# Optimization experiments

Hardware: AMD Instinct MI355X
Metric: run time of the kernel (lower is better)

Reference implementation:

```python
import jax, jax.numpy as jnp
import numpy as np

H, DK, DV, CHUNK = 4, 256, 256, 32

def _silu(x):
    return x * jax.nn.sigmoid(x)

def _l2norm(x, eps=1e-6):
    return x * jax.lax.rsqrt(jnp.sum(x * x, -1, keepdims=True) + eps)

def _rmsnorm(x, w, eps=1e-5):
    return x * jax.lax.rsqrt(jnp.mean(x * x, -1, keepdims=True) + eps) * w

def _causal_dwconv(x, w):
    # x: (B, L, C), w: (C, K) -> causal depthwise conv -> (B, L, C)
    C = x.shape[-1]
    K = w.shape[-1]
    xp = jnp.pad(x, ((0, 0), (K - 1, 0), (0, 0))).transpose(0, 2, 1)  # NCH
    y = jax.lax.conv_general_dilated(xp, w[:, None, :], (1,), 'VALID',
                                     feature_group_count=C,
                                     dimension_numbers=('NCH', 'OIH', 'NCH'))
    return y.transpose(0, 2, 1)

def _fir(x, filt):
    # x: (B, L, H, D), filt: (H, D, K) depthwise causal FIR per (head, channel)
    B, L, h, d = x.shape
    y = _causal_dwconv(x.reshape(B, L, h * d), filt.reshape(h * d, -1))
    return y.reshape(B, L, h, d)

def _delta_rule_chunkwise(q, k, v, beta):
    # q,k: (B,H,L,DK); v: (B,H,L,DV); beta: (B,H,L). L % CHUNK == 0.
    b, h, L, dk = q.shape
    dv = v.shape[-1]
    n = L // CHUNK
    q = _l2norm(q)
    k = _l2norm(k)
    v = v * beta[..., None]
    k_beta = k * beta[..., None]
    rs = lambda t: t.reshape(b, h, n, CHUNK, -1)
    q, k, v, k_beta = rs(q), rs(k), rs(v), rs(k_beta)
    eye = jnp.eye(CHUNK, dtype=q.dtype)
    strict_lower = jnp.tril(jnp.ones((CHUNK, CHUNK), bool), -1)
    A = jnp.where(strict_lower, jnp.einsum('bhncd,bhnsd->bhncs', k_beta, k), 0.0)
    # The torch row-wise loop computes (I + strict_lower(K_beta K^T))^{-1}
    attn_inv = jax.scipy.linalg.solve_triangular(eye + A, jnp.broadcast_to(eye, A.shape), lower=True)
    u = attn_inv @ v       # (b,h,n,c,dv)
    w = attn_inv @ k_beta  # (b,h,n,c,dk)
    incl_lower = jnp.tril(jnp.ones((CHUNK, CHUNK), bool))

    def step(S, inp):
        q_i, k_i, u_i, w_i = inp
        attn_local = jnp.where(incl_lower, q_i @ jnp.swapaxes(k_i, -1, -2), 0.0)
        u_t = u_i - w_i @ S
        o_i = q_i @ S + attn_local @ u_t
        return S + jnp.swapaxes(k_i, -1, -2) @ u_t, o_i

    S0 = jnp.zeros((b, h, dk, dv), q.dtype)
    xs = tuple(jnp.moveaxis(t, 2, 0) for t in (q, k, u, w))
    S, out = jax.lax.scan(step, S0, xs)
    return jnp.moveaxis(out, 0, 2).reshape(b, h, L, dv), S

def _stats(x):
    # per-branch head statistics over feature dim: mean, var, abs-mean, l2-norm
    return jnp.stack([x.mean(-1), x.var(-1), jnp.abs(x).mean(-1),
                      jnp.sqrt(jnp.sum(x * x, -1))], -1)

def _forward(x, Wq, Wk, Wv, Wb, conv_q, conv_k, conv_v, fir_long, fir_short,
             W1, b1, W2, b2, log_temp, base_bias, conv_residual_logit, rms_w, Wo):
    B, L, D = x.shape
    q = _silu(_causal_dwconv(x @ Wq, conv_q)).reshape(B, L, H, DK)
    k = _silu(_causal_dwconv(x @ Wk, conv_k)).reshape(B, L, H, DK)
    v = _silu(_causal_dwconv(x @ Wv, conv_v)).reshape(B, L, H, DV)
    beta = jax.nn.sigmoid(x @ Wb)  # (B, L, H)
    delta, _S = _delta_rule_chunkwise(q.transpose(0, 2, 1, 3), k.transpose(0, 2, 1, 3),
                                      v.transpose(0, 2, 1, 3), beta.transpose(0, 2, 1))
    delta = delta.transpose(0, 2, 1, 3)  # (B, L, H, DV)
    f_short = _fir(v, fir_short)
    f_long = _fir(v, fir_long)
    stats = jnp.concatenate([_stats(f_short), _stats(f_long), _stats(delta), _stats(v)], -1)
    hidden_exp = jnp.broadcast_to(x[:, :, None, :], (B, L, H, D))
    gate_in = jnp.concatenate([hidden_exp, stats], -1)  # (B,L,H,D+16)
    h1 = jax.nn.gelu(gate_in @ W1 + b1, approximate=False)
    logits = h1 @ W2 + b2 + base_bias  # (B, L, H, 4)
    temp = jax.nn.softplus(log_temp) + 1e-4
    p = jax.nn.softmax(logits / temp[:, None], -1)
    eps = 0.05  # step 0 -> alpha = 1 -> floor = floor_start
    p = jnp.maximum(p, jnp.array([eps, eps, 0.0, 0.0], p.dtype))
    p = p / jnp.sum(p, -1, keepdims=True)
    o = (p[..., 0:1] * f_short + p[..., 1:2] * f_long +
         p[..., 2:3] * delta + p[..., 3:4] * v)
    o = o + 0.5 * jax.nn.sigmoid(conv_residual_logit)[None, None, :, None] * f_short
    o = _rmsnorm(o, rms_w)
    return o.reshape(B, L, H * DV) @ Wo

def setup_inputs():
    key = jax.random.key(0)
    ks = jax.random.split(key, 13)
    B, L, D = 2, 2048, 1024
    f = jnp.float32
    n = lambda k, shape, s=0.02: jax.random.normal(k, shape, f) * s
    return {
        'x': jax.random.normal(ks[0], (B, L, D), f),
        'Wq': n(ks[1], (D, D)),
        'Wk': n(ks[2], (D, D)),
        'Wv': n(ks[3], (D, D)),
        'Wb': n(ks[4], (D, H)),
        'conv_q': n(ks[5], (D, 4), 0.1),
        'conv_k': n(ks[6], (D, 4), 0.1),
        'conv_v': n(ks[7], (D, 4), 0.1),
        'fir_long': n(ks[8], (H, DV, 64)),
        'fir_short': n(ks[9], (H, DV, 5)),
        'W1': n(ks[10], (D + 16, D)),
        'b1': jnp.zeros((D,), f),
        'W2': n(ks[11], (D, 4)),
        'b2': jnp.zeros((4,), f),
        'log_temp': jnp.full((H,), float(np.log(np.expm1(0.7))), f),
        'base_bias': jnp.tile(jnp.array([-0.5, -0.5, 1.0, 3.0], f), (H, 1)),
        'conv_residual_logit': jnp.full((H,), -2.0, f),
        'rms_w': jnp.ones((DV,), f),
        'Wo': n(ks[12], (D, D)),
    }

def reference(x, Wq, Wk, Wv, Wb, conv_q, conv_k, conv_v, fir_long, fir_short,
              W1, b1, W2, b2, log_temp, base_bias, conv_residual_logit, rms_w, Wo):
    return _forward(x, Wq, Wk, Wv, Wb, conv_q, conv_k, conv_v, fir_long, fir_short,
                    W1, b1, W2, b2, log_temp, base_bias, conv_residual_logit, rms_w, Wo)
```

## Files before the change

### kernel.cpp

```cpp
#include <hip/hip_runtime.h>
#include <math.h>

constexpr int NB = 2, NL = 2048, ND = 1024, NH = 4;
constexpr int NCHK = 64;
constexpr int NBL = NB * NL;
#define BLDSZ (NB * NL * ND)

constexpr int OPS_CH = 36864;
constexpr int STG_CH = 26624;

__device__ float g_v[BLDSZ];
__device__ float g_delta[BLDSZ];
__device__ float g_fs[BLDSZ];
__device__ float g_fl[BLDSZ];
__device__ float g_xw1[BLDSZ];
__device__ float g_beta[NBL * NH];
__device__ unsigned short g_qlb[BLDSZ];
__device__ unsigned short g_klb[BLDSZ];
__device__ unsigned short g_vlb[BLDSZ];
__device__ unsigned short g_ops[(size_t)8 * 64 * OPS_CH];
__device__ unsigned short g_xb[BLDSZ];
__device__ unsigned short g_omixb[BLDSZ];
__device__ unsigned short g_btw[5 * 1024 * 1024];

__device__ __forceinline__ float sigmoidf(float x) { return 1.f / (1.f + expf(-x)); }

__device__ __forceinline__ unsigned short f2bf(float f) {
  union { float f; unsigned int u; } v; v.f = f;
  unsigned int r = v.u + 0x7FFFu + ((v.u >> 16) & 1u);
  return (unsigned short)(r >> 16);
}
__device__ __forceinline__ float bf2f(unsigned int bits16) {
  union { unsigned int u; float f; } v; v.u = bits16 << 16; return v.f;
}
__device__ __forceinline__ unsigned int packbf(float a, float b) {
  return (unsigned int)f2bf(a) | ((unsigned int)f2bf(b) << 16);
}

typedef __attribute__((ext_vector_type(8))) short short8v;
typedef __attribute__((ext_vector_type(16))) float f32x16;

__device__ __forceinline__ unsigned int cvtpk(float lo, float hi) {
  unsigned int r;
  asm("v_cvt_pk_bf16_f32 %0, %1, %2" : "=v"(r) : "v"(lo), "v"(hi));
  return r;
}

__device__ __forceinline__ void mkfrag(const f32x16 v, short8v& fb0, short8v& fb1) {
  unsigned int P0 = cvtpk(v[0], v[1]),   P1 = cvtpk(v[2], v[3]);
  unsigned int P2 = cvtpk(v[4], v[5]),   P3 = cvtpk(v[6], v[7]);
  unsigned int P4 = cvtpk(v[8], v[9]),   P5 = cvtpk(v[10], v[11]);
  unsigned int P6 = cvtpk(v[12], v[13]), P7 = cvtpk(v[14], v[15]);
  asm("v_permlane32_swap_b32 %0, %1" : "+v"(P0), "+v"(P2));
  asm("v_permlane32_swap_b32 %0, %1" : "+v"(P1), "+v"(P3));
  asm("v_permlane32_swap_b32 %0, %1" : "+v"(P4), "+v"(P6));
  asm("v_permlane32_swap_b32 %0, %1" : "+v"(P5), "+v"(P7));
  unsigned int f0[4] = {P0, P1, P2, P3}, f1[4] = {P4, P5, P6, P7};
  fb0 = *(short8v*)f0; fb1 = *(short8v*)f1;
}

#define GLL16(SRC, DST)                                                                    \
  __builtin_amdgcn_global_load_lds(                                                        \
      (const __attribute__((address_space(1))) unsigned int*)(SRC),                        \
      (__attribute__((address_space(3))) unsigned int*)(DST), 16, 0, 0)

__device__ __forceinline__ void gemm128_core(const unsigned short* __restrict__ A,
                                             const unsigned short* __restrict__ Bt,
                                             int m0, int n0, int t,
                                             unsigned short* As, unsigned short* Bs,
                                             f32x16 acc[2][2]) {
  const int w = t >> 6, lane = t & 63, l31 = lane & 31, lhi = lane >> 5;
  const int wm = (w & 1) * 64, wn = (w >> 1) * 64;
#pragma unroll
  for (int mt = 0; mt < 2; ++mt)
#pragma unroll
    for (int nt = 0; nt < 2; ++nt)
#pragma unroll
      for (int e = 0; e < 16; ++e) acc[mt][nt][e] = 0.f;

  for (int k0 = 0; k0 < 1024; k0 += 64) {
#pragma unroll
    for (int i = 0; i < 4; ++i) {
      int sl = i * 4 + w;
      int srow = sl * 8 + (lane >> 3);
      int gc = (((lane & 7) ^ (srow & 7))) * 8;
      GLL16(A + (size_t)(m0 + srow) * 1024 + k0 + gc, &As[sl * 512]);
      GLL16(Bt + (size_t)(n0 + srow) * 1024 + k0 + gc, &Bs[sl * 512]);
    }
    __syncthreads();
#pragma unroll
    for (int ksl = 0; ksl < 4; ++ksl) {
      int kb = ksl * 2 + lhi;
      short8v af[2], bf[2];
#pragma unroll
      for (int mt = 0; mt < 2; ++mt) {
        int row = wm + mt * 32 + l31;
        af[mt] = *(const short8v*)&As[row * 64 + ((kb ^ (row & 7)) * 8)];
      }
#pragma unroll
      for (int nt = 0; nt < 2; ++nt) {
        int row = wn + nt * 32 + l31;
        bf[nt] = *(const short8v*)&Bs[row * 64 + ((kb ^ (row & 7)) * 8)];
      }
#pragma unroll
      for (int mt = 0; mt < 2; ++mt)
#pragma unroll
        for (int nt = 0; nt < 2; ++nt)
          acc[mt][nt] = __builtin_amdgcn_mfma_f32_32x32x16_bf16(af[mt], bf[nt], acc[mt][nt], 0, 0, 0);
    }
    __syncthreads();
  }
}

__global__ __launch_bounds__(256) void pack_all_kernel(const float* __restrict__ x,
                                                       const float* __restrict__ Wq,
                                                       const float* __restrict__ Wk,
                                                       const float* __restrict__ Wv,
                                                       const float* __restrict__ W1,
                                                       const float* __restrict__ Wo,
                                                       const float* __restrict__ Wb) {
  __shared__ float tile[64][65];
  int blk = blockIdx.x, t = threadIdx.x;
  if (blk < 2048) {
    int i8 = blk * 256 + t;
    const float* p = x + (size_t)i8 * 8;
    float4 a = *(const float4*)p;
    float4 b = *(const float4*)(p + 4);
    uint4 v;
    v.x = packbf(a.x, a.y); v.y = packbf(a.z, a.w);
    v.z = packbf(b.x, b.y); v.w = packbf(b.z, b.w);
    *(uint4*)&g_xb[(size_t)i8 * 8] = v;
    return;
  }
  if (blk < 3328) {
    int sel = (blk - 2048) >> 8, wb = (blk - 2048) & 255;
    const float* W = (sel == 0) ? Wq : (sel == 1) ? Wk : (sel == 2) ? Wv : (sel == 3) ? W1 : Wo;
    int bx = wb & 15, by = wb >> 4;
    int n0 = bx * 64, k0 = by * 64;
#pragma unroll
    for (int i = 0; i < 4; ++i) {
      int id = t + i * 256;
      int r = id >> 4, c4 = (id & 15) * 4;
      float4 v = *(const float4*)&W[(size_t)(k0 + r) * 1024 + n0 + c4];
      tile[r][c4 + 0] = v.x; tile[r][c4 + 1] = v.y; tile[r][c4 + 2] = v.z; tile[r][c4 + 3] = v.w;
    }
    __syncthreads();
    unsigned int* out = (unsigned int*)g_btw + (size_t)sel * 524288;
#pragma unroll
    for (int i = 0; i < 8; ++i) {
      int id = t + i * 256;
      int nn = id >> 5, ku = id & 31;
      out[(size_t)(n0 + nn) * 512 + (k0 >> 1) + ku] = packbf(tile[2 * ku][nn], tile[2 * ku + 1][nn]);
    }
    return;
  }
  int bl = blk - 3328;
  int h = t >> 6, lane = t & 63;
  const float* xr = x + (size_t)bl * ND;
  float acc = 0.f;
  for (int d = lane; d < ND; d += 64) acc += xr[d] * Wb[d * 4 + h];
#pragma unroll
  for (int off = 32; off; off >>= 1) acc += __shfl_xor(acc, off);
  if (lane == 0) g_beta[bl * 4 + h] = sigmoidf(acc);
}

__global__ __launch_bounds__(256) void qkv_gemm_kernel() {
  __shared__ unsigned short As[128 * 64];
  __shared__ unsigned short Bs[128 * 64];
  const int sel = blockIdx.x >> 8, hb = blockIdx.x & 255;
  const unsigned short* Bt = g_btw + (size_t)sel * 1024 * 1024;
  unsigned short* C = (sel == 0) ? g_qlb : (sel == 1) ? g_klb : g_vlb;
  const int m0 = (hb >> 3) * 128, n0 = (hb & 7) * 128;
  const int t = threadIdx.x;
  const int w = t >> 6, lane = t & 63, l31 = lane & 31, lhi = lane >> 5;
  const int wm = (w & 1) * 64, wn = (w >> 1) * 64;
  f32x16 acc[2][2];
  gemm128_core(g_xb, Bt, m0, n0, t, As, Bs, acc);
#pragma unroll
  for (int mt = 0; mt < 2; ++mt)
#pragma unroll
    for (int nt = 0; nt < 2; ++nt) {
      int col = n0 + wn + nt * 32 + l31;
#pragma unroll
      for (int e = 0; e < 16; ++e) {
        int row = m0 + wm + mt * 32 + (e & 3) + 8 * (e >> 2) + 4 * lhi;
        C[(size_t)row * 1024 + col] = f2bf(acc[mt][nt][e]);
      }
    }
}

__global__ __launch_bounds__(256) void convv_kernel(const float* __restrict__ cv) {
  int blk = blockIdx.x, t = threadIdx.x;
  int idx = blk * 256 + t;
  int c = idx & (ND - 1);
  int bl = idx >> 10;
  int l = bl & (NL - 1);
  float w0 = cv[c * 4 + 0], w1 = cv[c * 4 + 1], w2 = cv[c * 4 + 2], w3 = cv[c * 4 + 3];
  float acc = w3 * bf2f(g_vlb[(size_t)bl * ND + c]);
  if (l >= 1) acc += w2 * bf2f(g_vlb[(size_t)(bl - 1) * ND + c]);
  if (l >= 2) acc += w1 * bf2f(g_vlb[(size_t)(bl - 2) * ND + c]);
  if (l >= 3) acc += w0 * bf2f(g_vlb[(size_t)(bl - 3) * ND + c]);
  g_v[idx] = acc * sigmoidf(acc);
}

__global__ __launch_bounds__(256) void hgemm_out_kernel(float* __restrict__ Cext) {
  __shared__ unsigned short As[128 * 64];
  __shared__ unsigned short Bs[128 * 64];
  const int m0 = (blockIdx.x >> 3) * 128, n0 = (blockIdx.x & 7) * 128;
  const int t = threadIdx.x;
  const int w = t >> 6, lane = t & 63, l31 = lane & 31, lhi = lane >> 5;
  const int wm = (w & 1) * 64, wn = (w >> 1) * 64;
  f32x16 acc[2][2];
  gemm128_core(g_omixb, g_btw + (size_t)4 * 1024 * 1024, m0, n0, t, As, Bs, acc);
#pragma unroll
  for (int mt = 0; mt < 2; ++mt)
#pragma unroll
    for (int nt = 0; nt < 2; ++nt) {
      int col = n0 + wn + nt * 32 + l31;
#pragma unroll
      for (int e = 0; e < 16; ++e) {
        int row = m0 + wm + mt * 32 + (e & 3) + 8 * (e >> 2) + 4 * lhi;
        Cext[(size_t)row * 1024 + col] = acc[mt][nt][e];
      }
    }
}

__global__ __launch_bounds__(256) void delta_prep_kernel(const float* __restrict__ cq,
                                                         const float* __restrict__ ck) {
  __shared__ float X[32][260];
  __shared__ float Y[32][260];
  __shared__ float Am[32][33];
  __shared__ float Tm[32][33];
  __shared__ float bet[32];
  int blk = blockIdx.x;
  int n = blk & 63, h = (blk >> 6) & 3, b = blk >> 8;
  int t = threadIdx.x;
  size_t rowbase = (size_t)(b * NL + n * 32);
  size_t obase = (size_t)blk * OPS_CH;
  const int st_ = t >> 5, j_ = (t >> 4) & 1, lh_ = (t >> 3) & 1, e_ = t & 7;
  const int l31_ = t & 31;

  {
    const int hcol = h * 256 + t;
    const unsigned short* qp = g_qlb + hcol;
    const unsigned short* kp = g_klb + hcol;
    float wq0 = cq[hcol * 4 + 0], wq1 = cq[hcol * 4 + 1], wq2 = cq[hcol * 4 + 2], wq3 = cq[hcol * 4 + 3];
    float wk0 = ck[hcol * 4 + 0], wk1 = ck[hcol * 4 + 1], wk2 = ck[hcol * 4 + 2], wk3 = ck[hcol * 4 + 3];
    float qa = 0.f, qb_ = 0.f, qc = 0.f, ka = 0.f, kb_ = 0.f, kc = 0.f;
    if (n > 0) {
      qa = bf2f(qp[(rowbase - 3) * 1024]); qb_ = bf2f(qp[(rowbase - 2) * 1024]); qc = bf2f(qp[(rowbase - 1) * 1024]);
      ka = bf2f(kp[(rowbase - 3) * 1024]); kb_ = bf2f(kp[(rowbase - 2) * 1024]); kc = bf2f(kp[(rowbase - 1) * 1024]);
    }
#pragma unroll 4
    for (int r = 0; r < 32; ++r) {
      float qd = bf2f(qp[(rowbase + r) * 1024]);
      float kd = bf2f(kp[(rowbase + r) * 1024]);
      float aq = wq3 * qd + wq2 * qc + wq1 * qb_ + wq0 * qa;
      float ak = wk3 * kd + wk2 * kc + wk1 * kb_ + wk0 * ka;
      X[r][t] = aq * sigmoidf(aq);
      Y[r][t] = ak * sigmoidf(ak);
      qa = qb_; qb_ = qc; qc = qd;
      ka = kb_; kb_ = kc; kc = kd;
    }
  }
  if (t < 32) bet[t] = g_beta[(rowbase + t) * 4 + h];
  __syncthreads();

  {
    int wv = t >> 6, lane = t & 63;
    int r = wv * 8 + (lane >> 3), sub = lane & 7;
    float sq = 0.f, sk = 0.f;
#pragma unroll
    for (int m4 = 0; m4 < 8; ++m4) {
      float4 a = *(const float4*)&X[r][sub * 32 + m4 * 4];
      float4 bb = *(const float4*)&Y[r][sub * 32 + m4 * 4];
      sq += a.x * a.x + a.y * a.y + a.z * a.z + a.w * a.w;
      sk += bb.x * bb.x + bb.y * bb.y + bb.z * bb.z + bb.w * bb.w;
    }
    sq += __shfl_xor(sq, 1); sq += __shfl_xor(sq, 2); sq += __shfl_xor(sq, 4);
    sk += __shfl_xor(sk, 1); sk += __shfl_xor(sk, 2); sk += __shfl_xor(sk, 4);
    float rq = rsqrtf(sq + 1e-6f), rk = rsqrtf(sk + 1e-6f);
#pragma unroll
    for (int m4 = 0; m4 < 8; ++m4) {
      float4 a = *(const float4*)&X[r][sub * 32 + m4 * 4];
      a.x *= rq; a.y *= rq; a.z *= rq; a.w *= rq;
      *(float4*)&X[r][sub * 32 + m4 * 4] = a;
      float4 bb = *(const float4*)&Y[r][sub * 32 + m4 * 4];
      bb.x *= rk; bb.y *= rk; bb.z *= rk; bb.w *= rk;
      *(float4*)&Y[r][sub * 32 + m4 * 4] = bb;
    }
  }
  __syncthreads();

  if (t < 64) {
    const int al = t & 31, ah = t >> 5;
    f32x16 Cat;
#pragma unroll
    for (int e = 0; e < 16; ++e) Cat[e] = 0.f;
#pragma unroll
    for (int st = 0; st < 16; ++st) {
      int kb = st * 16 + ah * 8;
      float4 a0 = *(const float4*)&X[al][kb], a1 = *(const float4*)&X[al][kb + 4];
      float4 b0 = *(const float4*)&Y[al][kb], b1 = *(const float4*)&Y[al][kb + 4];
      unsigned int af[4] = {cvtpk(a0.x, a0.y), cvtpk(a0.z, a0.w), cvtpk(a1.x, a1.y), cvtpk(a1.z, a1.w)};
      unsigned int bf_[4] = {cvtpk(b0.x, b0.y), cvtpk(b0.z, b0.w), cvtpk(b1.x, b1.y), cvtpk(b1.z, b1.w)};
      Cat = __builtin_amdgcn_mfma_f32_32x32x16_bf16(*(short8v*)af, *(short8v*)bf_, Cat, 0, 0, 0);
    }
#pragma unroll
    for (int e = 0; e < 16; ++e) {
      int row = (e & 3) + 8 * (e >> 2) + 4 * ah, col = al;
      float v = (col <= row) ? Cat[e] : 0.f;
      g_ops[obase + 32768 + (size_t)(((col >> 4) * 64) + ((col >> 3) & 1) * 32 + row) * 8 + (col & 7)] = f2bf(v);
    }
  }

  {
    size_t qb = obase + 8192 + (size_t)(((st_ * 2 + j_) * 64) + lh_ * 32) * 8 + e_;
#pragma unroll 8
    for (int r = 0; r < 32; ++r)
      g_ops[qb + r * 8] = f2bf(X[r][t]);
#pragma unroll
    for (int j = 0; j < 2; ++j)
#pragma unroll
      for (int lh = 0; lh < 2; ++lh) {
        int kr0 = j * 16 + lh * 8;
        uint4 v;
        v.x = packbf(Y[kr0 + 0][t], Y[kr0 + 1][t]);
        v.y = packbf(Y[kr0 + 2][t], Y[kr0 + 3][t]);
        v.z = packbf(Y[kr0 + 4][t], Y[kr0 + 5][t]);
        v.w = packbf(Y[kr0 + 6][t], Y[kr0 + 7][t]);
        *(uint4*)&g_ops[obase + 16384 + (size_t)(((st_ * 2 + j) * 64) + lh * 32 + l31_) * 8] = v;
      }
  }
  __syncthreads();

#pragma unroll
  for (int i = 0; i < 8; ++i) {
    int j = t + i * 256;
    int r = j >> 6, d4 = (j & 63) << 2;
    float be = bet[r];
    float4 bb = *(const float4*)&Y[r][d4];
    bb.x *= be; bb.y *= be; bb.z *= be; bb.w *= be;
    *(float4*)&X[r][d4] = bb;
  }
  __syncthreads();

  if (t < 64) {
    const int al = t & 31, ah = t >> 5;
    f32x16 Cam;
#pragma unroll
    for (int e = 0; e < 16; ++e) Cam[e] = 0.f;
#pragma unroll
    for (int st = 0; st < 16; ++st) {
      int kb = st * 16 + ah * 8;
      float4 a0 = *(const float4*)&X[al][kb], a1 = *(const float4*)&X[al][kb + 4];
      float4 b0 = *(const float4*)&Y[al][kb], b1 = *(const float4*)&Y[al][kb + 4];
      unsigned int af[4] = {cvtpk(a0.x, a0.y), cvtpk(a0.z, a0.w), cvtpk(a1.x, a1.y), cvtpk(a1.z, a1.w)};
      unsigned int bf_[4] = {cvtpk(b0.x, b0.y), cvtpk(b0.z, b0.w), cvtpk(b1.x, b1.y), cvtpk(b1.z, b1.w)};
      Cam = __builtin_amdgcn_mfma_f32_32x32x16_bf16(*(short8v*)af, *(short8v*)bf_, Cam, 0, 0, 0);
    }
#pragma unroll
    for (int e = 0; e < 16; ++e) {
      int row = (e & 3) + 8 * (e >> 2) + 4 * ah, col = al;
      if (col < row) Am[row][col] = Cam[e];
    }
  }
  __syncthreads();

  if (t < 32) {
    const int j = t;
#pragma unroll
    for (int i = 0; i < 32; ++i) {
      float a = (i == j) ? 1.f : 0.f;
#pragma unroll
      for (int m = 0; m < i; ++m) {
        float p = Am[i][m] * Tm[m][j];
        a -= (m >= j) ? p : 0.f;
      }
      Tm[i][j] = a;
    }
  }
  __syncthreads();

  {
    float acc[32];
#pragma unroll
    for (int r = 0; r < 32; ++r) acc[r] = 0.f;
#pragma unroll
    for (int m = 0; m < 32; ++m) {
      float xv = X[m][t];
#pragma unroll
      for (int r = m; r < 32; ++r) acc[r] += Tm[r][m] * xv;
    }
    size_t wb = obase + (size_t)(((st_ * 2 + j_) * 64) + lh_ * 32) * 8 + e_;
#pragma unroll 8
    for (int r = 0; r < 32; ++r)
      g_ops[wb + r * 8] = f2bf(acc[r]);
  }
#pragma unroll
  for (int i = 0; i < 8; ++i) {
    int j = t + i * 256;
    int r = j >> 6, d4 = (j & 63) << 2;
    size_t gi = (rowbase + r) * ND + h * 256 + d4;
    float be = bet[r];
    float4 vv = *(const float4*)&g_v[gi];
    vv.x *= be; vv.y *= be; vv.z *= be; vv.w *= be;
    *(float4*)&Y[r][d4] = vv;
  }
  __syncthreads();

  {
    float acc[32];
#pragma unroll
    for (int r = 0; r < 32; ++r) acc[r] = 0.f;
#pragma unroll
    for (int m = 0; m < 32; ++m) {
      float yv = Y[m][t];
#pragma unroll
      for (int r = m; r < 32; ++r) acc[r] += Tm[r][m] * yv;
    }
    int q = t >> 5;
#pragma unroll
    for (int g = 0; g < 4; ++g)
#pragma unroll
      for (int lh = 0; lh < 2; ++lh) {
        int kr0 = 8 * g + 4 * lh;
        uint2 v;
        v.x = packbf(acc[kr0 + 0], acc[kr0 + 1]);
        v.y = packbf(acc[kr0 + 2], acc[kr0 + 3]);
        *(uint2*)&g_ops[obase + 24576 + (size_t)(((q * 4 + g) * 64) + lh * 32 + l31_) * 4] = v;
      }
  }
}

__global__ __launch_bounds__(256, 1) void scan_fir_kernel(const float* __restrict__ firl,
                                                          const float* __restrict__ firs) {
  __shared__ __align__(16) unsigned char smem[2 * STG_CH * 2];
  const int blk = blockIdx.x;
  const int t = threadIdx.x;

  if (blk < 64) {
    if (t >= 64) return;
    unsigned short (*buf)[STG_CH] = (unsigned short (*)[STG_CH])smem;
    const int bh = blk & 7;
    const int b = bh >> 2, h = bh & 3;
    const int s = blk >> 3;
    const int lane = t;
    const int l31 = lane & 31, lhi = lane >> 5;

    f32x16 Sacc[8];
#pragma unroll
    for (int st = 0; st < 8; ++st)
#pragma unroll
      for (int e = 0; e < 16; ++e) Sacc[st][e] = 0.f;

    const unsigned short* ops = g_ops + (size_t)bh * 64 * OPS_CH;
    const int fo = lane * 8;
    const int utg = 24576 + s * 1024;

#define STAGE_CHUNK(SRC, DST)                                                              \
    {                                                                                      \
      const unsigned short* sp = (SRC);                                                    \
      unsigned short* dp = (DST);                                                          \
      _Pragma("unroll")                                                                    \
      for (int k = 0; k < 48; ++k)                                                         \
        GLL16(sp + (size_t)k * 512 + fo, dp + k * 512);                                    \
      _Pragma("unroll")                                                                    \
      for (int k = 0; k < 2; ++k) {                                                        \
        GLL16(sp + utg + (size_t)k * 512 + fo, dp + 24576 + k * 512);                      \
        GLL16(sp + 32768 + (size_t)k * 512 + fo, dp + 25600 + k * 512);                    \
      }                                                                                    \
    }

    STAGE_CHUNK(ops, &buf[0][0]);

    for (int n = 0; n < 64; ++n) {
      const int cur = n & 1;
      if (n == 0) asm volatile("s_waitcnt vmcnt(0)" ::: "memory");
      else        asm volatile("s_waitcnt vmcnt(16)" ::: "memory");

      if (n < 63) STAGE_CHUNK(ops + (size_t)(n + 1) * OPS_CH, &buf[cur ^ 1][0]);

      const unsigned short* Lb = &buf[cur][0];
      f32x16 wuA, wuB, ooA, ooB;
#pragma unroll
      for (int e = 0; e < 16; ++e) { wuA[e] = 0.f; wuB[e] = 0.f; ooA[e] = 0.f; ooB[e] = 0.f; }

#pragma unroll
      for (int st = 0; st < 8; ++st) {
        short8v s0, s1;
        mkfrag(Sacc[st], s0, s1);
        short8v wa0 = *(const short8v*)&Lb[(st * 2 + 0) * 512 + fo];
        short8v wa1 = *(const short8v*)&Lb[(st * 2 + 1) * 512 + fo];
        short8v qa0 = *(const short8v*)&Lb[8192 + (st * 2 + 0) * 512 + fo];
        short8v qa1 = *(const short8v*)&Lb[8192 + (st * 2 + 1) * 512 + fo];
        wuA = __builtin_amdgcn_mfma_f32_32x32x16_bf16(wa0, s0, wuA, 0, 0, 0);
        wuB = __builtin_amdgcn_mfma_f32_32x32x16_bf16(wa1, s1, wuB, 0, 0, 0);
        ooA = __builtin_amdgcn_mfma_f32_32x32x16_bf16(qa0, s0, ooA, 0, 0, 0);
        ooB = __builtin_amdgcn_mfma_f32_32x32x16_bf16(qa1, s1, ooB, 0, 0, 0);
      }

      f32x16 ut;
#pragma unroll
      for (int g = 0; g < 4; ++g) {
        uint2 uu = *(const uint2*)&Lb[24576 + ((g * 64) + lhi * 32 + l31) * 4];
        ut[4 * g + 0] = bf2f(uu.x & 0xffffu) - wuA[4 * g + 0] - wuB[4 * g + 0];
        ut[4 * g + 1] = bf2f(uu.x >> 16)     - wuA[4 * g + 1] - wuB[4 * g + 1];
        ut[4 * g + 2] = bf2f(uu.y & 0xffffu) - wuA[4 * g + 2] - wuB[4 * g + 2];
        ut[4 * g + 3] = bf2f(uu.y >> 16)     - wuA[4 * g + 3] - wuB[4 * g + 3];
      }
      short8v u0, u1;
      mkfrag(ut, u0, u1);

      {
        short8v aa0 = *(const short8v*)&Lb[25600 + 0 * 512 + fo];
        short8v aa1 = *(const short8v*)&Lb[25600 + 1 * 512 + fo];
        ooA = __builtin_amdgcn_mfma_f32_32x32x16_bf16(aa0, u0, ooA, 0, 0, 0);
        ooB = __builtin_amdgcn_mfma_f32_32x32x16_bf16(aa1, u1, ooB, 0, 0, 0);
      }
#pragma unroll
      for (int st = 0; st < 8; ++st) {
        short8v ka0 = *(const short8v*)&Lb[16384 + (st * 2 + 0) * 512 + fo];
        short8v ka1 = *(const short8v*)&Lb[16384 + (st * 2 + 1) * 512 + fo];
        Sacc[st] = __builtin_amdgcn_mfma_f32_32x32x16_bf16(ka0, u0, Sacc[st], 0, 0, 0);
        Sacc[st] = __builtin_amdgcn_mfma_f32_32x32x16_bf16(ka1, u1, Sacc[st], 0, 0, 0);
      }

      size_t ob = ((size_t)(b * NL + n * 32)) * ND + h * 256 + s * 32 + l31;
#pragma unroll
      for (int e = 0; e < 16; ++e) {
        int row = (e & 3) + 8 * (e >> 2) + 4 * lhi;
        g_delta[ob + (size_t)row * ND] = ooA[e] + ooB[e];
      }
    }
#undef STAGE_CHUNK
  } else if (blk < 64 + 512) {
    float (*ft)[257] = (float (*)[257])smem;
    int fb_ = blk - 64;
    int cbk = fb_ & 3, lb = (fb_ >> 2) & 63, b = fb_ >> 8;
    int c = cbk * 256 + t;
    const float* fbp = firl + (size_t)cbk * 256 * 64;
#pragma unroll 4
    for (int i = 0; i < 64; ++i) {
      int j = t + i * 256;
      ft[j & 63][j >> 6] = fbp[j];
    }
    __syncthreads();
    float ff[64];
#pragma unroll
    for (int i = 0; i < 64; ++i) ff[i] = ft[i][t];
    float acc[32];
#pragma unroll
    for (int i = 0; i < 32; ++i) acc[i] = 0.f;
    const float* vb = g_v + (size_t)b * NL * ND + c;
    const int l0 = lb * 32;
#pragma unroll
    for (int d = 0; d < 95; ++d) {
      int lr = l0 - 63 + d;
      float vv = (lr >= 0) ? vb[(size_t)lr * ND] : 0.f;
      const int lo = (d > 63) ? (d - 63) : 0;
      const int hi = (d < 31) ? d : 31;
#pragma unroll
      for (int li = lo; li <= hi; ++li) acc[li] += ff[d - li] * vv;
    }
    float* ob = g_fl + ((size_t)(b * NL + l0)) * ND + c;
#pragma unroll
    for (int li = 0; li < 32; ++li) ob[(size_t)li * ND] = acc[li];
  } else if (blk < 64 + 512 + BLDSZ / 1024) {
    int idx4 = (blk - 576) * 256 + t;
    int c4 = idx4 & 255;
    int bl = idx4 >> 8;
    int l = bl & (NL - 1);
    float fw[4][5];
#pragma unroll
    for (int j = 0; j < 4; ++j)
#pragma unroll
      for (int tap = 0; tap < 5; ++tap) fw[j][tap] = firs[(c4 * 4 + j) * 5 + tap];
    float4 acc = {0.f, 0.f, 0.f, 0.f};
    const float4* v4 = (const float4*)g_v;
#pragma unroll
    for (int tap = 0; tap < 5; ++tap) {
      int ls = l + tap - 4;
      if (ls >= 0) {
        float4 vv = v4[(size_t)(bl + tap - 4) * 256 + c4];
        acc.x += fw[0][tap] * vv.x; acc.y += fw[1][tap] * vv.y;
        acc.z += fw[2][tap] * vv.z; acc.w += fw[3][tap] * vv.w;
      }
    }
    ((float4*)g_fs)[(size_t)bl * 256 + c4] = acc;
  } else {
    unsigned short* As = (unsigned short*)smem;
    unsigned short* Bs = (unsigned short*)smem + 8192;
    int hb = blk - (64 + 512 + BLDSZ / 1024);
    const int m0 = (hb >> 3) * 128, n0 = (hb & 7) * 128;
    const int w = t >> 6, lane = t & 63, l31 = lane & 31, lhi = lane >> 5;
    const int wm = (w & 1) * 64, wn = (w >> 1) * 64;
    f32x16 acc[2][2];
    gemm128_core(g_xb, g_btw + (size_t)3 * 1024 * 1024, m0, n0, t, As, Bs, acc);
#pragma unroll
    for (int mt = 0; mt < 2; ++mt)
#pragma unroll
      for (int nt = 0; nt < 2; ++nt) {
        int col = n0 + wn + nt * 32 + l31;
#pragma unroll
        for (int e = 0; e < 16; ++e) {
          int row = m0 + wm + mt * 32 + (e & 3) + 8 * (e >> 2) + 4 * lhi;
          g_xw1[(size_t)row * 1024 + col] = acc[mt][nt][e];
        }
      }
  }
}

__global__ __launch_bounds__(256) void tail_kernel(const float* __restrict__ W1,
                                                   const float* __restrict__ b1,
                                                   const float* __restrict__ W2,
                                                   const float* __restrict__ b2,
                                                   const float* __restrict__ log_temp,
                                                   const float* __restrict__ base_bias,
                                                   const float* __restrict__ crl,
                                                   const float* __restrict__ rms_w) {
  __shared__ float st[4][16];
  __shared__ float red[4][4];
  __shared__ float pl[4][4];
  int bl = blockIdx.x, t = threadIdx.x;
  int h = t >> 6, lane = t & 63;

  {
    size_t base = (size_t)bl * ND + h * 256 + lane * 4;
#pragma unroll
    for (int br = 0; br < 4; ++br) {
      const float* p = (br == 0) ? g_fs : (br == 1) ? g_fl : (br == 2) ? g_delta : g_v;
      float4 x4 = *(const float4*)&p[base];
      float s = x4.x + x4.y + x4.z + x4.w;
      float s2 = x4.x * x4.x + x4.y * x4.y + x4.z * x4.z + x4.w * x4.w;
      float sa = fabsf(x4.x) + fabsf(x4.y) + fabsf(x4.z) + fabsf(x4.w);
#pragma unroll
      for (int off = 32; off; off >>= 1) {
        s += __shfl_xor(s, off);
        s2 += __shfl_xor(s2, off);
        sa += __shfl_xor(sa, off);
      }
      if (lane == 0) {
        float mean = s * (1.f / 256.f);
        st[h][br * 4 + 0] = mean;
        st[h][br * 4 + 1] = s2 * (1.f / 256.f) - mean * mean;
        st[h][br * 4 + 2] = sa * (1.f / 256.f);
        st[h][br * 4 + 3] = sqrtf(s2);
      }
    }
  }
  __syncthreads();

  const float* W1s = W1 + 1024 * 1024;
  for (int hh = 0; hh < 4; ++hh) {
    float sv[16];
#pragma unroll
    for (int s = 0; s < 16; ++s) sv[s] = st[hh][s];
    float a0 = 0.f, a1 = 0.f, a2 = 0.f, a3 = 0.f;
    for (int j = t; j < 1024; j += 256) {
      float val = g_xw1[(size_t)bl * 1024 + j] + b1[j];
#pragma unroll
      for (int s = 0; s < 16; ++s) val += sv[s] * W1s[s * 1024 + j];
      float gg = 0.5f * val * (1.f + erff(val * 0.70710678118654752f));
      float4 w2 = *(const float4*)&W2[j * 4];
      a0 += gg * w2.x; a1 += gg * w2.y; a2 += gg * w2.z; a3 += gg * w2.w;
    }
#pragma unroll
    for (int off = 32; off; off >>= 1) {
      a0 += __shfl_xor(a0, off); a1 += __shfl_xor(a1, off);
      a2 += __shfl_xor(a2, off); a3 += __shfl_xor(a3, off);
    }
    if (lane == 0) { red[h][0] = a0; red[h][1] = a1; red[h][2] = a2; red[h][3] = a3; }
    __syncthreads();
    if (t == 0) {
      float lg[4];
#pragma unroll
      for (int m = 0; m < 4; ++m)
        lg[m] = red[0][m] + red[1][m] + red[2][m] + red[3][m] + b2[m] + base_bias[hh * 4 + m];
      float lt = log_temp[hh];
      float sp = (lt > 20.f) ? lt : log1pf(expf(lt));
      float inv = 1.f / (sp + 1e-4f);
      float z0 = lg[0] * inv, z1 = lg[1] * inv, z2 = lg[2] * inv, z3 = lg[3] * inv;
      float mx = fmaxf(fmaxf(z0, z1), fmaxf(z2, z3));
      float e0 = expf(z0 - mx), e1 = expf(z1 - mx), e2 = expf(z2 - mx), e3 = expf(z3 - mx);
      float si = 1.f / (e0 + e1 + e2 + e3);
      float p0 = e0 * si, p1 = e1 * si, p2 = e2 * si, p3 = e3 * si;
      p0 = fmaxf(p0, 0.05f); p1 = fmaxf(p1, 0.05f);
      float s2i = 1.f / (p0 + p1 + p2 + p3);
      p0 *= s2i; p1 *= s2i; p2 *= s2i; p3 *= s2i;
      p0 += 0.5f * sigmoidf(crl[hh]);
      pl[hh][0] = p0; pl[hh][1] = p1; pl[hh][2] = p2; pl[hh][3] = p3;
    }
    __syncthreads();
  }

  float p0 = pl[h][0], p1 = pl[h][1], p2 = pl[h][2], p3 = pl[h][3];
  size_t base = (size_t)bl * ND + h * 256 + lane * 4;
  float4 a = *(const float4*)&g_fs[base];
  float4 bb = *(const float4*)&g_fl[base];
  float4 c = *(const float4*)&g_delta[base];
  float4 d = *(const float4*)&g_v[base];
  float o0 = p0 * a.x + p1 * bb.x + p2 * c.x + p3 * d.x;
  float o1 = p0 * a.y + p1 * bb.y + p2 * c.y + p3 * d.y;
  float o2 = p0 * a.z + p1 * bb.z + p2 * c.z + p3 * d.z;
  float o3 = p0 * a.w + p1 * bb.w + p2 * c.w + p3 * d.w;
  float s2 = o0 * o0 + o1 * o1 + o2 * o2 + o3 * o3;
#pragma unroll
  for (int off = 32; off; off >>= 1) s2 += __shfl_xor(s2, off);
  float rms = rsqrtf(s2 * (1.f / 256.f) + 1e-5f);
  float4 w4 = *(const float4*)&rms_w[lane * 4];
  uint2 pw;
  pw.x = packbf(o0 * rms * w4.x, o1 * rms * w4.y);
  pw.y = packbf(o2 * rms * w4.z, o3 * rms * w4.w);
  *(uint2*)&g_omixb[base] = pw;
}

extern "C" void kernel_launch(void* const* d_in, const int* in_sizes, int n_in,
                              void* d_out, int out_size, void* d_ws, size_t ws_size,
                              hipStream_t stream) {
  const float* x = (const float*)d_in[0];
  const float* Wq = (const float*)d_in[1];
  const float* Wk = (const float*)d_in[2];
  const float* Wv = (const float*)d_in[3];
  const float* Wb = (const float*)d_in[4];
  const float* cq = (const float*)d_in[5];
  const float* ck = (const float*)d_in[6];
  const float* cv = (const float*)d_in[7];
  const float* firl = (const float*)d_in[8];
  const float* firs = (const float*)d_in[9];
  const float* W1 = (const float*)d_in[10];
  const float* b1 = (const float*)d_in[11];
  const float* W2 = (const float*)d_in[12];
  const float* b2 = (const float*)d_in[13];
  const float* ltp = (const float*)d_in[14];
  const float* bbs = (const float*)d_in[15];
  const float* crl = (const float*)d_in[16];
  const float* rw = (const float*)d_in[17];
  const float* Wo = (const float*)d_in[18];
  float* out = (float*)d_out;

  dim3 blk(256);
  pack_all_kernel<<<2048 + 5 * 256 + NBL, blk, 0, stream>>>(x, Wq, Wk, Wv, W1, Wo, Wb);
  qkv_gemm_kernel<<<768, blk, 0, stream>>>();
  convv_kernel<<<16384, blk, 0, stream>>>(cv);
  delta_prep_kernel<<<NB * NH * NCHK, blk, 0, stream>>>(cq, ck);
  scan_fir_kernel<<<64 + 512 + BLDSZ / 1024 + 256, blk, 0, stream>>>(firl, firs);
  tail_kernel<<<NBL, blk, 0, stream>>>(W1, b1, W2, b2, ltp, bbs, crl, rw);
  hgemm_out_kernel<<<256, blk, 0, stream>>>(out);
}
```

Before: 386.8 us.

## Swizzle GEMM block order and give each wavefront one head in tail gating

The QKV and output GEMMs remap block indices so consecutive blocks walk down M within one N column, aiming for better L2 reuse of the weight tile. The tail kernel drops the serial four-head loop with its two block barriers per head. Each wavefront now computes its own head's gate MLP and softmax independently over all 1024 hidden units, leaving a single barrier. This removes barriers and idle threads but gives each wave four times the loop iterations of the old per-head split.

```diff
diff --git a/kernel.cpp b/kernel.cpp
--- a/kernel.cpp
+++ b/kernel.cpp
@@ -167,7 +167,9 @@
 __global__ __launch_bounds__(256) void qkv_gemm_kernel() {
   __shared__ unsigned short As[128 * 64];
   __shared__ unsigned short Bs[128 * 64];
-  const int sel = blockIdx.x >> 8, hb = blockIdx.x & 255;
+  const int sel = blockIdx.x >> 8;
+  const int hb0 = blockIdx.x & 255;
+  const int hb = (hb0 & 7) * 32 + (hb0 >> 3);
   const unsigned short* Bt = g_btw + (size_t)sel * 1024 * 1024;
   unsigned short* C = (sel == 0) ? g_qlb : (sel == 1) ? g_klb : g_vlb;
   const int m0 = (hb >> 3) * 128, n0 = (hb & 7) * 128;
@@ -206,7 +208,8 @@
 __global__ __launch_bounds__(256) void hgemm_out_kernel(float* __restrict__ Cext) {
   __shared__ unsigned short As[128 * 64];
   __shared__ unsigned short Bs[128 * 64];
-  const int m0 = (blockIdx.x >> 3) * 128, n0 = (blockIdx.x & 7) * 128;
+  const int hb = (blockIdx.x & 7) * 32 + (blockIdx.x >> 3);
+  const int m0 = (hb >> 3) * 128, n0 = (hb & 7) * 128;
   const int t = threadIdx.x;
   const int w = t >> 6, lane = t & 63, l31 = lane & 31, lhi = lane >> 5;
   const int wm = (w & 1) * 64, wn = (w >> 1) * 64;
@@ -620,7 +623,6 @@
                                                    const float* __restrict__ crl,
                                                    const float* __restrict__ rms_w) {
   __shared__ float st[4][16];
-  __shared__ float red[4][4];
   __shared__ float pl[4][4];
   int bl = blockIdx.x, t = threadIdx.x;
   int h = t >> 6, lane = t & 63;
@@ -651,13 +653,13 @@
   }
   __syncthreads();
 
-  const float* W1s = W1 + 1024 * 1024;
-  for (int hh = 0; hh < 4; ++hh) {
+  {
+    const float* W1s = W1 + 1024 * 1024;
     float sv[16];
 #pragma unroll
-    for (int s = 0; s < 16; ++s) sv[s] = st[hh][s];
+    for (int s = 0; s < 16; ++s) sv[s] = st[h][s];
     float a0 = 0.f, a1 = 0.f, a2 = 0.f, a3 = 0.f;
-    for (int j = t; j < 1024; j += 256) {
+    for (int j = lane; j < 1024; j += 64) {
       float val = g_xw1[(size_t)bl * 1024 + j] + b1[j];
 #pragma unroll
       for (int s = 0; s < 16; ++s) val += sv[s] * W1s[s * 1024 + j];
@@ -670,14 +672,10 @@
       a0 += __shfl_xor(a0, off); a1 += __shfl_xor(a1, off);
       a2 += __shfl_xor(a2, off); a3 += __shfl_xor(a3, off);
     }
-    if (lane == 0) { red[h][0] = a0; red[h][1] = a1; red[h][2] = a2; red[h][3] = a3; }
-    __syncthreads();
-    if (t == 0) {
-      float lg[4];
-#pragma unroll
-      for (int m = 0; m < 4; ++m)
-        lg[m] = red[0][m] + red[1][m] + red[2][m] + red[3][m] + b2[m] + base_bias[hh * 4 + m];
-      float lt = log_temp[hh];
+    if (lane == 0) {
+      float lg[4] = {a0 + b2[0] + base_bias[h * 4 + 0], a1 + b2[1] + base_bias[h * 4 + 1],
+                     a2 + b2[2] + base_bias[h * 4 + 2], a3 + b2[3] + base_bias[h * 4 + 3]};
+      float lt = log_temp[h];
       float sp = (lt > 20.f) ? lt : log1pf(expf(lt));
       float inv = 1.f / (sp + 1e-4f);
       float z0 = lg[0] * inv, z1 = lg[1] * inv, z2 = lg[2] * inv, z3 = lg[3] * inv;
@@ -688,11 +686,11 @@
       p0 = fmaxf(p0, 0.05f); p1 = fmaxf(p1, 0.05f);
       float s2i = 1.f / (p0 + p1 + p2 + p3);
       p0 *= s2i; p1 *= s2i; p2 *= s2i; p3 *= s2i;
-      p0 += 0.5f * sigmoidf(crl[hh]);
-      pl[hh][0] = p0; pl[hh][1] = p1; pl[hh][2] = p2; pl[hh][3] = p3;
-    }
-    __syncthreads();
-  }
+      p0 += 0.5f * sigmoidf(crl[h]);
+      pl[h][0] = p0; pl[h][1] = p1; pl[h][2] = p2; pl[h][3] = p3;
+    }
+  }
+  __syncthreads();
 
   float p0 = pl[h][0], p1 = pl[h][1], p2 = pl[h][2], p3 = pl[h][3];
   size_t base = (size_t)bl * ND + h * 256 + lane * 4;
```

New measurement: 383.2 us. Within noise of the previous version (-0.9%).
